# Optimization experiments

Measured on AMD Instinct MI355X. Metric: run time of the kernel, lower is better.

## Reference

```python
import jax, jax.numpy as jnp
import numpy as np

B, T, D = 512, 200, 512

def setup_inputs() -> dict:
    key = jax.random.key(0)
    k1, k2, k3 = jax.random.split(key, 3)
    inputs = jax.random.normal(k1, (B, T, D), dtype=jnp.float32)
    # Keras 'uniform' initializer -> U(-0.05, 0.05)
    W = jax.random.uniform(k2, (T, T), minval=-0.05, maxval=0.05, dtype=jnp.float32)
    b = jax.random.uniform(k3, (T,), minval=-0.05, maxval=0.05, dtype=jnp.float32)
    return {"inputs": inputs, "W": W, "b": b}

def reference(inputs, W, b):
    # x = permute(inputs, (0,2,1)) -> [B, D, T]; scores over timestep axis
    # a = softmax(tanh(x @ W + b)) along last axis (T)
    scores = jnp.tanh(jnp.einsum('btd,ts->bds', inputs, W) + b)  # [B, D, T]
    a = jax.nn.softmax(scores, axis=-1)                           # softmax over T
    # permute back to [B, T, D], elementwise multiply, sum over T -> [B, D]
    out = jnp.einsum('bdt,btd->bd', a, inputs)
    return out
```

## Files before the change

### kernel.cpp

```cpp
#include <hip/hip_runtime.h>
#include <cstdint>
#include <cstddef>

#define B_DIM 512
#define T_DIM 200
#define D_DIM 512
#define NPAD  208
#define NKG   28
#define NT    13
#define KS_STEPS 7
#define SLICE 3208

typedef short  short8  __attribute__((ext_vector_type(8)));
typedef float  floatx4 __attribute__((ext_vector_type(4)));

__device__ __forceinline__ unsigned short f2bf(float f) {
  unsigned int u = __float_as_uint(f);
  u += 0x7fffu + ((u >> 16) & 1u);
  return (unsigned short)(u >> 16);
}
__device__ __forceinline__ float bf2f(unsigned short h) {
  return __uint_as_float(((unsigned int)h) << 16);
}
__device__ __forceinline__ unsigned int cvt_pk_bf16(float a, float b) {
  unsigned int d;
  asm("v_cvt_pk_bf16_f32 %0, %1, %2" : "=v"(d) : "v"(a), "v"(b));
  return d;
}

__global__ void prep_w_kernel(const float* __restrict__ W,
                              unsigned short* __restrict__ wf) {
  int idx = blockIdx.x * blockDim.x + threadIdx.x;
  if (idx >= NKG * 8 * NPAD) return;
  int k = idx / NPAD;
  int n = idx - k * NPAD;
  float v = (k < T_DIM && n < T_DIM) ? W[k * T_DIM + n] : 0.0f;
  wf[((size_t)(k >> 3) * NPAD + n) * 8 + (k & 7)] = f2bf(v);
}

__global__ __launch_bounds__(256, 4)
void attn_kernel(const float* __restrict__ X,
                 const unsigned short* __restrict__ wf,
                 const float* __restrict__ bias,
                 float* __restrict__ out) {
  __shared__ __align__(16) unsigned short Xs[4 * SLICE];
  __shared__ __align__(16) float comb[4][64][2];

  const int tid  = threadIdx.x;
  const int wv   = tid >> 6;
  const int lane = tid & 63;
  const int l15  = lane & 15;
  const int g    = lane >> 4;

  const int bid  = blockIdx.x;
  const int bb   = bid >> 3;
  const int dblk = (bid & 7) << 6;

  {
    const float* xb = X + (size_t)bb * (T_DIM * D_DIM) + dblk;
    #pragma unroll
    for (int it = 0; it < 13; ++it) {
      int i = it * 256 + tid;
      if (it < 12 || tid < 128) {
        int t  = i >> 4;
        int c4 = i & 15;
        float4 v = *(const float4*)(xb + (size_t)t * D_DIM + (c4 << 2));
        unsigned short* dst = Xs + (c4 >> 2) * SLICE
                            + ((t >> 3) * 16 + ((c4 & 3) << 2)) * 8 + (t & 7);
        unsigned int w01 = cvt_pk_bf16(v.x, v.y);
        unsigned int w23 = cvt_pk_bf16(v.z, v.w);
        dst[0]  = (unsigned short)(w01 & 0xffffu);
        dst[8]  = (unsigned short)(w01 >> 16);
        dst[16] = (unsigned short)(w23 & 0xffffu);
        dst[24] = (unsigned short)(w23 >> 16);
      }
    }
  }
  __syncthreads();

  const int nt0 = (wv == 0) ? 0 : (1 + 3 * wv);
  const int ntw = (wv == 0) ? 4 : 3;

  floatx4 acc[4][4];
  #pragma unroll
  for (int h = 0; h < 4; ++h)
    #pragma unroll
    for (int j = 0; j < 4; ++j)
      acc[h][j] = (floatx4){0.f, 0.f, 0.f, 0.f};

  const unsigned short* wk = wf + ((size_t)g * NPAD + nt0 * 16 + l15) * 8;

  #pragma unroll
  for (int ks = 0; ks < KS_STEPS; ++ks) {
    const int kg = ks * 4 + g;
    short8 b[4];
    #pragma unroll
    for (int j = 0; j < 4; ++j)
      if (j < ntw) b[j] = *(const short8*)(wk + (size_t)ks * (4 * NPAD * 8) + j * 128);
    const bool av = (ks < 6) || (g == 0);
    short8 a[4];
    #pragma unroll
    for (int h = 0; h < 4; ++h)
      a[h] = av ? *(const short8*)&Xs[h * SLICE + (kg * 16 + l15) * 8]
                : (short8){0, 0, 0, 0, 0, 0, 0, 0};
    #pragma unroll
    for (int j = 0; j < 4; ++j)
      if (j < ntw) {
        #pragma unroll
        for (int h = 0; h < 4; ++h)
          acc[h][j] = __builtin_amdgcn_mfma_f32_16x16x32_bf16(a[h], b[j], acc[h][j], 0, 0, 0);
      }
  }

  float part[4][4], rs[4][4];
  #pragma unroll
  for (int h = 0; h < 4; ++h)
    #pragma unroll
    for (int r = 0; r < 4; ++r) { part[h][r] = 0.f; rs[h][r] = 0.f; }

  #pragma unroll
  for (int j = 0; j < 4; ++j) {
    if (j < ntw) {
      const int nt = nt0 + j;
      const int t  = nt * 16 + l15;
      const bool valid = (t < T_DIM);
      const int tc = valid ? t : (T_DIM - 1);
      const float bvn = bias[tc];
      const unsigned short* xp = &Xs[((tc >> 3) * 16) * 8 + (tc & 7)];
      #pragma unroll
      for (int r = 0; r < 4; ++r) {
        const int m = g * 4 + r;
        #pragma unroll
        for (int h = 0; h < 4; ++h) {
          float z  = acc[h][j][r] + bvn;
          float e  = __expf(2.0f * z);
          float th = 1.0f - __fdividef(2.0f, e + 1.0f);
          float p  = valid ? __expf(th) : 0.0f;
          rs[h][r]   += p;
          part[h][r] += p * bf2f(xp[h * SLICE + m * 8]);
        }
      }
    }
  }
  #pragma unroll
  for (int off = 1; off <= 8; off <<= 1)
    #pragma unroll
    for (int h = 0; h < 4; ++h)
      #pragma unroll
      for (int r = 0; r < 4; ++r) {
        part[h][r] += __shfl_xor(part[h][r], off, 16);
        rs[h][r]   += __shfl_xor(rs[h][r],   off, 16);
      }

  if (l15 == 0) {
    #pragma unroll
    for (int h = 0; h < 4; ++h)
      #pragma unroll
      for (int r = 0; r < 4; ++r) {
        comb[wv][h * 16 + g * 4 + r][0] = part[h][r];
        comb[wv][h * 16 + g * 4 + r][1] = rs[h][r];
      }
  }
  __syncthreads();

  if (tid < 64) {
    float ps = 0.f, ss = 0.f;
    #pragma unroll
    for (int w = 0; w < 4; ++w) {
      ps += comb[w][tid][0];
      ss += comb[w][tid][1];
    }
    out[(size_t)bb * D_DIM + dblk + tid] = ps * __frcp_rn(ss);
  }
}

extern "C" void kernel_launch(void* const* d_in, const int* in_sizes, int n_in,
                              void* d_out, int out_size, void* d_ws, size_t ws_size,
                              hipStream_t stream) {
  const float* X  = (const float*)d_in[0];
  const float* W  = (const float*)d_in[1];
  const float* bs = (const float*)d_in[2];
  float* out = (float*)d_out;
  unsigned short* wf = (unsigned short*)d_ws;

  const int wtot = NKG * 8 * NPAD;
  hipLaunchKernelGGL(prep_w_kernel, dim3((wtot + 255) / 256), dim3(256), 0, stream,
                     W, wf);
  hipLaunchKernelGGL(attn_kernel, dim3(4096), dim3(256), 0, stream,
                     X, wf, bs, out);
}
```

Measured before the change: 317.7 us.

## Simplify tanh-exp math, trim shuffle reduction, hoist load addressing, rebalance tiles

Measured after the change: 315.3 us. No clear change (-0.8%).

```diff
diff --git a/kernel.cpp b/kernel.cpp
--- a/kernel.cpp
+++ b/kernel.cpp
@@ -44,7 +44,7 @@
                  const float* __restrict__ bias,
                  float* __restrict__ out) {
   __shared__ __align__(16) unsigned short Xs[4 * SLICE];
-  __shared__ __align__(16) float comb[4][64][2];
+  __shared__ __align__(16) float comb[4][4][64][2];
 
   const int tid  = threadIdx.x;
   const int wv   = tid >> 6;
@@ -58,15 +58,15 @@
 
   {
     const float* xb = X + (size_t)bb * (T_DIM * D_DIM) + dblk;
+    const int c4 = tid & 15;
+    const int t0 = tid >> 4;
+    const float* src = xb + (size_t)t0 * D_DIM + (c4 << 2);
+    unsigned short* dst = Xs + (c4 >> 2) * SLICE
+                        + ((t0 >> 3) * 16 + ((c4 & 3) << 2)) * 8 + (t0 & 7);
     #pragma unroll
     for (int it = 0; it < 13; ++it) {
-      int i = it * 256 + tid;
       if (it < 12 || tid < 128) {
-        int t  = i >> 4;
-        int c4 = i & 15;
-        float4 v = *(const float4*)(xb + (size_t)t * D_DIM + (c4 << 2));
-        unsigned short* dst = Xs + (c4 >> 2) * SLICE
-                            + ((t >> 3) * 16 + ((c4 & 3) << 2)) * 8 + (t & 7);
+        float4 v = *(const float4*)src;
         unsigned int w01 = cvt_pk_bf16(v.x, v.y);
         unsigned int w23 = cvt_pk_bf16(v.z, v.w);
         dst[0]  = (unsigned short)(w01 & 0xffffu);
@@ -74,12 +74,14 @@
         dst[16] = (unsigned short)(w23 & 0xffffu);
         dst[24] = (unsigned short)(w23 >> 16);
       }
+      src += 16 * D_DIM;
+      dst += 256;
     }
   }
   __syncthreads();
 
-  const int nt0 = (wv == 0) ? 0 : (1 + 3 * wv);
-  const int ntw = (wv == 0) ? 4 : 3;
+  const int nt0 = 3 * wv;
+  const int ntw = 3 + (wv == 3);
 
   floatx4 acc[4][4];
   #pragma unroll
@@ -125,17 +127,17 @@
       const int t  = nt * 16 + l15;
       const bool valid = (t < T_DIM);
       const int tc = valid ? t : (T_DIM - 1);
-      const float bvn = bias[tc];
+      const float bb2 = 2.0f * bias[tc];
       const unsigned short* xp = &Xs[((tc >> 3) * 16) * 8 + (tc & 7)];
       #pragma unroll
       for (int r = 0; r < 4; ++r) {
         const int m = g * 4 + r;
         #pragma unroll
         for (int h = 0; h < 4; ++h) {
-          float z  = acc[h][j][r] + bvn;
-          float e  = __expf(2.0f * z);
-          float th = 1.0f - __fdividef(2.0f, e + 1.0f);
-          float p  = valid ? __expf(th) : 0.0f;
+          float u  = __expf(__builtin_fmaf(acc[h][j][r], 2.0f, bb2));
+          float v  = __fdividef(2.0f, u + 1.0f);
+          float p0 = __expf(-v);
+          float p  = valid ? p0 : 0.0f;
           rs[h][r]   += p;
           part[h][r] += p * bf2f(xp[h * SLICE + m * 8]);
         }
@@ -143,7 +145,7 @@
     }
   }
   #pragma unroll
-  for (int off = 1; off <= 8; off <<= 1)
+  for (int off = 1; off <= 2; off <<= 1)
     #pragma unroll
     for (int h = 0; h < 4; ++h)
       #pragma unroll
@@ -152,13 +154,15 @@
         rs[h][r]   += __shfl_xor(rs[h][r],   off, 16);
       }
 
-  if (l15 == 0) {
+  if ((l15 & 3) == 0) {
+    const int q = l15 >> 2;
     #pragma unroll
     for (int h = 0; h < 4; ++h)
       #pragma unroll
       for (int r = 0; r < 4; ++r) {
-        comb[wv][h * 16 + g * 4 + r][0] = part[h][r];
-        comb[wv][h * 16 + g * 4 + r][1] = rs[h][r];
+        const int idx = h * 16 + g * 4 + r;
+        comb[wv][q][idx][0] = part[h][r];
+        comb[wv][q][idx][1] = rs[h][r];
       }
   }
   __syncthreads();
@@ -166,10 +170,13 @@
   if (tid < 64) {
     float ps = 0.f, ss = 0.f;
     #pragma unroll
-    for (int w = 0; w < 4; ++w) {
-      ps += comb[w][tid][0];
-      ss += comb[w][tid][1];
-    }
+    for (int w = 0; w < 4; ++w)
+      #pragma unroll
+      for (int q = 0; q < 4; ++q) {
+        const float2 v = *(const float2*)&comb[w][q][tid][0];
+        ps += v.x;
+        ss += v.y;
+      }
     out[(size_t)bb * D_DIM + dblk + tid] = ps * __frcp_rn(ss);
   }
 }
```
